# Kernel optimization log

Measured on AMD Instinct MI355X. Metric: run time of the kernel, lower is better.

The kernel has to match this reference:

```python
import jax, jax.numpy as jnp
import numpy as np

B, T, D, H = 4, 1024, 2048, 16
E = D // H  # head_dim = 128


def setup_inputs() -> dict:
    key = jax.random.key(0)
    ks = jax.random.split(key, 10)
    s = 1.0 / np.sqrt(D)
    x = jax.random.normal(ks[0], (B, T, D), dtype=jnp.float32)
    attention_mask = jnp.ones((B, T), dtype=jnp.int32)
    # Per-head q/k/v projections stacked along head axis: [H, E, D] weights, [H, E] biases.
    Wq = jax.random.uniform(ks[1], (H, E, D), jnp.float32, -s, s)
    bq = jax.random.uniform(ks[2], (H, E), jnp.float32, -s, s)
    Wk = jax.random.uniform(ks[3], (H, E, D), jnp.float32, -s, s)
    bk = jax.random.uniform(ks[4], (H, E), jnp.float32, -s, s)
    Wv = jax.random.uniform(ks[5], (H, E, D), jnp.float32, -s, s)
    bv = jax.random.uniform(ks[6], (H, E), jnp.float32, -s, s)
    Wo = jax.random.uniform(ks[7], (D, D), jnp.float32, -s, s)
    bo = jax.random.uniform(ks[8], (D,), jnp.float32, -s, s)
    return {"x": x, "attention_mask": attention_mask, "Wq": Wq, "bq": bq,
            "Wk": Wk, "bk": bk, "Wv": Wv, "bv": bv, "Wo": Wo, "bo": bo}


def _causal_mask(Tq, Tk, dtype):
    neg = jnp.finfo(dtype).min
    qi = jnp.arange(Tq)[:, None]
    ki = jnp.arange(Tk)[None, :]
    max_allowed = Tk - Tq + qi
    return jnp.where(ki > max_allowed, neg, jnp.zeros((), dtype)).astype(dtype)


def reference(x, attention_mask, Wq, bq, Wk, bk, Wv, bv, Wo, bo):
    dt = x.dtype
    neg = jnp.finfo(dt).min
    scale = 1.0 / np.sqrt(E)
    # per-head projections (vectorized over heads): [B,H,T,E]
    q = jnp.einsum('btd,hed->bhte', x, Wq) + bq[None, :, None, :]
    k = jnp.einsum('btd,hed->bhte', x, Wk) + bk[None, :, None, :]
    v = jnp.einsum('btd,hed->bhte', x, Wv) + bv[None, :, None, :]
    # scores [B,H,Tq,Tk]
    scores = jnp.einsum('bhqe,bhke->bhqk', q, k) * scale
    scores = scores + _causal_mask(T, T, dt)[None, None]
    keep = attention_mask.astype(bool)  # [B,Tk]
    scores = jnp.where(keep[:, None, None, :], scores, neg)
    probs = jax.nn.softmax(scores, axis=-1)
    y = jnp.einsum('bhqk,bhke->bhqe', probs, v)  # [B,H,T,E]
    # heads concatenated along feature dim in head order
    y = jnp.transpose(y, (0, 2, 1, 3)).reshape(B, T, D)
    out = y @ Wo.T + bo
    return out
```

## Files before the change

### kernel.cpp

```cpp
#include <hip/hip_runtime.h>
#include <hip/hip_bf16.h>


typedef __attribute__((ext_vector_type(4))) float f32x4;
typedef __attribute__((ext_vector_type(8))) short s16x8;
typedef __attribute__((ext_vector_type(4))) unsigned short us16x4;
typedef __attribute__((ext_vector_type(8))) unsigned short us16x8;

#define Td 1024
#define Dd 2048
#define SCALE 0.08838834764831845f

__device__ __forceinline__ unsigned short f2bf(float f) {
  unsigned int u = __builtin_bit_cast(unsigned int, f);
  u = (u + 0x7fffu + ((u >> 16) & 1u)) >> 16;
  return (unsigned short)u;
}

__device__ __forceinline__ void gload_lds16(const void* g, void* l) {
  __builtin_amdgcn_global_load_lds(
      (const __attribute__((address_space(1))) unsigned int*)g,
      (__attribute__((address_space(3))) unsigned int*)l, 16, 0, 0);
}

__global__ void cvt_f32_bf16(const float* __restrict__ in,
                             unsigned short* __restrict__ out, int n4) {
  int i = blockIdx.x * 256 + threadIdx.x;
  if (i >= n4) return;
  float4 v = reinterpret_cast<const float4*>(in)[i];
  us16x4 o = {f2bf(v.x), f2bf(v.y), f2bf(v.z), f2bf(v.w)};
  reinterpret_cast<us16x4*>(out)[i] = o;
}

__global__ void bias_concat(const float* __restrict__ bq, const float* __restrict__ bk,
                            const float* __restrict__ bv, float* __restrict__ out) {
  int i = blockIdx.x * 256 + threadIdx.x;
  const float* s = (i < 2048) ? bq : ((i < 4096) ? bk : bv);
  out[i] = s[i & 2047];
}

__global__ void prep_mask(const int* __restrict__ amask, unsigned* __restrict__ pmask) {
  const int b = blockIdx.x, tid = threadIdx.x;
  const int w = tid >> 6, lane = tid & 63;
#pragma unroll
  for (int j = 0; j < 4; ++j) {
    const int k = j * 256 + tid;
    unsigned long long ball = __ballot(amask[b * Td + k] != 0);
    if (lane == 0) {
      pmask[b * 32 + j * 8 + w * 2] = (unsigned)ball;
      pmask[b * 32 + j * 8 + w * 2 + 1] = (unsigned)(ball >> 32);
    }
  }
}

template <int MODE>
__global__ __launch_bounds__(256, 2) void gemm_bt(
    const unsigned short* __restrict__ A, const unsigned short* __restrict__ Bm,
    const float* __restrict__ bias, void* __restrict__ C,
    unsigned short* __restrict__ Cv, int M, int N, int K, int ldc) {
  __shared__ unsigned short As[8192];
  __shared__ unsigned short Bs[8192];
  const int tid = threadIdx.x;
  const int lane = tid & 63, w = tid >> 6;
  const int g = lane >> 4, m15 = lane & 15;
  const int wr = w >> 1, wc = w & 1;
  const int row0 = blockIdx.y * 128, col0 = blockIdx.x * 128;

  f32x4 acc[4][4] = {};
  const int nK = K >> 6;
  for (int kt = 0; kt < nK; ++kt) {
    const int k0 = kt << 6;
    __syncthreads();
#pragma unroll
    for (int i = 0; i < 4; ++i) {
      const int p = w * 256 + i * 64 + lane;
      const int prow = p >> 3;
      const int lslot = (p & 7) ^ (prow & 7);
      gload_lds16(A + (size_t)(row0 + prow) * K + k0 + lslot * 8,
                  &As[(size_t)(w * 256 + i * 64) * 8]);
      gload_lds16(Bm + (size_t)(col0 + prow) * K + k0 + lslot * 8,
                  &Bs[(size_t)(w * 256 + i * 64) * 8]);
    }
    __syncthreads();
#pragma unroll
    for (int ks = 0; ks < 2; ++ks) {
      s16x8 af[4], bf[4];
#pragma unroll
      for (int i = 0; i < 4; ++i) {
        const int r = wr * 64 + i * 16 + m15;
        af[i] = *reinterpret_cast<const s16x8*>(&As[(r * 8 + ((ks * 4 + g) ^ (r & 7))) * 8]);
      }
#pragma unroll
      for (int j = 0; j < 4; ++j) {
        const int r = wc * 64 + j * 16 + m15;
        bf[j] = *reinterpret_cast<const s16x8*>(&Bs[(r * 8 + ((ks * 4 + g) ^ (r & 7))) * 8]);
      }
#pragma unroll
      for (int i = 0; i < 4; ++i)
#pragma unroll
        for (int j = 0; j < 4; ++j)
          acc[i][j] = __builtin_amdgcn_mfma_f32_16x16x32_bf16(af[i], bf[j], acc[i][j], 0, 0, 0);
    }
  }
  if (MODE == 1 && col0 >= 4096) {
    const int vc0 = col0 - 4096;
#pragma unroll
    for (int j = 0; j < 4; ++j) {
      const int vcol = vc0 + wc * 64 + j * 16 + m15;
      const float bv = bias[4096 + vcol];
      const int hh = vcol >> 7, e = vcol & 127;
#pragma unroll
      for (int i = 0; i < 4; ++i) {
        const int row = row0 + wr * 64 + i * 16 + g * 4;
        const int bb = row >> 10, tt = row & 1023;
        us16x4 pk;
#pragma unroll
        for (int r = 0; r < 4; ++r) pk[r] = f2bf(acc[i][j][r] + bv);
        *reinterpret_cast<us16x4*>(&Cv[((size_t)((bb * 16 + hh) * 128 + e)) * Td + tt]) = pk;
      }
    }
  } else {
#pragma unroll
    for (int j = 0; j < 4; ++j) {
      const int col = col0 + wc * 64 + j * 16 + m15;
      const float bv = bias[col];
#pragma unroll
      for (int i = 0; i < 4; ++i)
#pragma unroll
        for (int r = 0; r < 4; ++r) {
          const int row = row0 + wr * 64 + i * 16 + g * 4 + r;
          const float v = acc[i][j][r] + bv;
          if (MODE)
            ((unsigned short*)C)[(size_t)row * ldc + col] = f2bf(v);
          else
            ((float*)C)[(size_t)row * ldc + col] = v;
        }
    }
  }
}

#define SOFTMAX_GRP(SV, G, QB, BND)                                              \
  {                                                                              \
    const int q = (QB) + m15;                                                    \
    float pv[16];                                                                \
    if (!(BND) && (pm0 & pm1) == 0xffffffffu) {                                  \
      _Pragma("unroll") for (int kc = 0; kc < 4; ++kc)                           \
          _Pragma("unroll") for (int r = 0; r < 4; ++r)                          \
              pv[kc * 4 + r] = SV[kc][r] * SCALE;                                \
    } else {                                                                     \
      _Pragma("unroll") for (int kc = 0; kc < 4; ++kc)                           \
          _Pragma("unroll") for (int r = 0; r < 4; ++r) {                        \
        const int kl = kc * 16 + g * 4 + r;                                      \
        const unsigned pmw = (kl < 32) ? pm0 : pm1;                              \
        const bool ok = ((pmw >> (kl & 31)) & 1u) && (k0 + kl <= q);             \
        pv[kc * 4 + r] = ok ? SV[kc][r] * SCALE : -3.0e38f;                      \
      }                                                                          \
    }                                                                            \
    float t0 = fmaxf(fmaxf(pv[0], pv[1]), fmaxf(pv[2], pv[3]));                  \
    float t1 = fmaxf(fmaxf(pv[4], pv[5]), fmaxf(pv[6], pv[7]));                  \
    float t2 = fmaxf(fmaxf(pv[8], pv[9]), fmaxf(pv[10], pv[11]));                \
    float t3 = fmaxf(fmaxf(pv[12], pv[13]), fmaxf(pv[14], pv[15]));              \
    float t = fmaxf(fmaxf(t0, t1), fmaxf(t2, t3));                               \
    t = fmaxf(t, __shfl_xor(t, 16));                                             \
    t = fmaxf(t, __shfl_xor(t, 32));                                             \
    const float mn = fmaxf(m_[G], t);                                            \
    const float al = __expf(m_[G] - mn);                                         \
    m_[G] = mn;                                                                  \
    float rs = 0.f;                                                              \
    _Pragma("unroll") for (int j = 0; j < 16; ++j) {                             \
      pv[j] = __expf(pv[j] - mn);                                                \
      rs += pv[j];                                                               \
    }                                                                            \
    rs += __shfl_xor(rs, 16);                                                    \
    rs += __shfl_xor(rs, 32);                                                    \
    l_[G] = l_[G] * al + rs;                                                     \
    _Pragma("unroll") for (int n = 0; n < 8; ++n) yt[G][n] *= al;                \
    _Pragma("unroll") for (int kc = 0; kc < 4; ++kc) {                           \
      us16x4 pk;                                                                 \
      _Pragma("unroll") for (int r = 0; r < 4; ++r) pk[r] = f2bf(pv[kc * 4 + r]);\
      const int ch = kc * 2 + (g >> 1);                                          \
      const int idx = (G) * 1024 + m15 * 64 + ((ch ^ (m15 & 7)) << 3) + (g & 1) * 4; \
      *reinterpret_cast<us16x4*>(&pw[idx]) = pk;                                 \
    }                                                                            \
  }

__global__ __launch_bounds__(512, 2) void attn(
    const unsigned short* __restrict__ qk, const unsigned short* __restrict__ vt,
    const unsigned* __restrict__ pmask, unsigned short* __restrict__ Y) {
  __shared__ unsigned short Ks[2][8192];
  __shared__ unsigned short Vs[2][8192];
  __shared__ unsigned short Ps[8][2048];
  const int d = blockIdx.x;
  const int slot = d >> 3;
  const int bh = (d & 7) * 8 + (slot >> 2);
  const int p = slot & 3;
  const int b = bh >> 4, h = bh & 15;
  const int ta = p, tb = 7 - p;
  const int tid = threadIdx.x, lane = tid & 63, w = tid >> 6;
  const int g = lane >> 4, m15 = lane & 15;
  const int qa = ta * 128 + w * 16, qb = tb * 128 + w * 16;
  unsigned short* pw = Ps[w];

  const unsigned short* qkb = qk + (size_t)b * Td * 4096;
  const unsigned short* vbb = vt + (size_t)bh * 128 * Td;

  s16x8 qf[2][4];
#pragma unroll
  for (int G = 0; G < 2; ++G) {
    const int q_ = G ? qb : qa;
#pragma unroll
    for (int c = 0; c < 4; ++c)
      qf[G][c] = *reinterpret_cast<const s16x8*>(
          &qkb[(size_t)(q_ + m15) * 4096 + h * 128 + c * 32 + g * 8]);
  }

  f32x4 yt[2][8] = {};
  float m_[2] = {-3.0e38f, -3.0e38f}, l_[2] = {0.f, 0.f};

  auto stage = [&](int buf, int kt) {
    const int k0s = kt << 6;
#pragma unroll
    for (int i = 0; i < 2; ++i) {
      const int pc = i * 512 + tid;
      const int kr = pc >> 4, ch = pc & 15;
      const int ls = ch ^ (kr & 7);
      gload_lds16(qkb + (size_t)(k0s + kr) * 4096 + 2048 + h * 128 + ls * 8,
                  &Ks[buf][(i * 512 + w * 64) * 8]);
      const int e = pc >> 3, cv = pc & 7;
      const int vs = cv ^ (e & 7);
      gload_lds16(vbb + (size_t)e * Td + k0s + vs * 8,
                  &Vs[buf][(i * 512 + w * 64) * 8]);
    }
  };

  const int nA = 2 * ta + 2, nB = 2 * tb + 2;
  stage(0, 0);
  asm volatile("s_waitcnt vmcnt(0)" ::: "memory");
  __syncthreads();
  int cur = 0;
  for (int kt = 0; kt < nB; ++kt) {
    const int k0 = kt << 6;
    const bool actA = kt < nA;
    if (kt + 1 < nB) stage(cur ^ 1, kt + 1);
    const unsigned pm0 = pmask[b * 32 + kt * 2];
    const unsigned pm1 = pmask[b * 32 + kt * 2 + 1];

    f32x4 s0[4] = {}, s1[4] = {};
    __builtin_amdgcn_s_setprio(1);
#pragma unroll
    for (int kc = 0; kc < 4; ++kc) {
      const int krow = kc * 16 + m15;
#pragma unroll
      for (int c = 0; c < 4; ++c) {
        const s16x8 kf = *reinterpret_cast<const s16x8*>(
            &Ks[cur][krow * 128 + (((c * 4 + g) ^ (krow & 7))) * 8]);
        if (actA) s0[kc] = __builtin_amdgcn_mfma_f32_16x16x32_bf16(kf, qf[0][c], s0[kc], 0, 0, 0);
        s1[kc] = __builtin_amdgcn_mfma_f32_16x16x32_bf16(kf, qf[1][c], s1[kc], 0, 0, 0);
      }
    }
    __builtin_amdgcn_s_setprio(0);

    if (actA) SOFTMAX_GRP(s0, 0, qa, kt >= 2 * ta)
    SOFTMAX_GRP(s1, 1, qb, kt >= 2 * tb)

    asm volatile("s_waitcnt lgkmcnt(0)" ::: "memory");
    __builtin_amdgcn_sched_barrier(0);
    s16x8 pf0[2], pf1[2];
#pragma unroll
    for (int kcc = 0; kcc < 2; ++kcc) {
      if (actA)
        pf0[kcc] = *reinterpret_cast<const s16x8*>(
            &pw[m15 * 64 + (((kcc * 4 + g) ^ (m15 & 7))) * 8]);
      pf1[kcc] = *reinterpret_cast<const s16x8*>(
          &pw[1024 + m15 * 64 + (((kcc * 4 + g) ^ (m15 & 7))) * 8]);
    }

    __builtin_amdgcn_s_setprio(1);
#pragma unroll
    for (int nt = 0; nt < 8; ++nt) {
      const int e = nt * 16 + m15;
#pragma unroll
      for (int kcc = 0; kcc < 2; ++kcc) {
        const s16x8 vf = *reinterpret_cast<const s16x8*>(
            &Vs[cur][e * 64 + (((kcc * 4 + g) ^ (e & 7))) * 8]);
        if (actA) yt[0][nt] = __builtin_amdgcn_mfma_f32_16x16x32_bf16(vf, pf0[kcc], yt[0][nt], 0, 0, 0);
        yt[1][nt] = __builtin_amdgcn_mfma_f32_16x16x32_bf16(vf, pf1[kcc], yt[1][nt], 0, 0, 0);
      }
    }
    __builtin_amdgcn_s_setprio(0);

    asm volatile("s_waitcnt vmcnt(0)" ::: "memory");
    __syncthreads();
    cur ^= 1;
  }

#pragma unroll
  for (int G = 0; G < 2; ++G) {
    const int q_ = G ? qb : qa;
    const float inv = 1.0f / l_[G];
#pragma unroll
    for (int half = 0; half < 2; ++half) {
#pragma unroll
      for (int ntl = 0; ntl < 4; ++ntl) {
        const int nt = half * 4 + ntl;
        us16x4 pk;
#pragma unroll
        for (int r = 0; r < 4; ++r) pk[r] = f2bf(yt[G][nt][r] * inv);
        const int slot8 = ntl * 4 + g;
        const int idx = m15 * 64 + (((slot8 >> 1) ^ (m15 & 7))) * 8 + (slot8 & 1) * 4;
        *reinterpret_cast<us16x4*>(&pw[idx]) = pk;
      }
      asm volatile("s_waitcnt lgkmcnt(0)" ::: "memory");
      __builtin_amdgcn_sched_barrier(0);
      const int qq = lane >> 2, c4 = lane & 3;
#pragma unroll
      for (int rr = 0; rr < 2; ++rr) {
        const int pr = c4 + rr * 4;
        us16x8 vv = *reinterpret_cast<const us16x8*>(&pw[qq * 64 + ((pr ^ (qq & 7))) * 8]);
        *reinterpret_cast<us16x8*>(
            &Y[(size_t)(b * Td + q_ + qq) * Dd + h * 128 + half * 64 + pr * 8]) = vv;
      }
      asm volatile("s_waitcnt lgkmcnt(0)" ::: "memory");
      __builtin_amdgcn_sched_barrier(0);
    }
  }
}

extern "C" void kernel_launch(void* const* d_in, const int* in_sizes, int n_in,
                              void* d_out, int out_size, void* d_ws, size_t ws_size,
                              hipStream_t stream) {
  const float* x = (const float*)d_in[0];
  const int* amask = (const int*)d_in[1];
  const float* Wq = (const float*)d_in[2];
  const float* bq = (const float*)d_in[3];
  const float* Wk = (const float*)d_in[4];
  const float* bk = (const float*)d_in[5];
  const float* Wv = (const float*)d_in[6];
  const float* bv = (const float*)d_in[7];
  const float* Wo = (const float*)d_in[8];
  const float* bo = (const float*)d_in[9];
  float* out = (float*)d_out;

  char* ws = (char*)d_ws;
  unsigned short* wqkv = (unsigned short*)(ws);
  unsigned short* xbf  = (unsigned short*)(ws + 25165824);
  unsigned short* qk   = (unsigned short*)(ws + 41943040);
  unsigned short* vt   = (unsigned short*)(ws + 75497472);
  unsigned short* wobf = (unsigned short*)(ws + 92274688);
  float* bqkv          = (float*)(ws + 100663296);
  unsigned short* ybuf = xbf;
  unsigned* pmask      = (unsigned*)ws;

  cvt_f32_bf16<<<8192, 256, 0, stream>>>(x, xbf, 2097152);
  cvt_f32_bf16<<<4096, 256, 0, stream>>>(Wq, wqkv, 1048576);
  cvt_f32_bf16<<<4096, 256, 0, stream>>>(Wk, wqkv + 4194304, 1048576);
  cvt_f32_bf16<<<4096, 256, 0, stream>>>(Wv, wqkv + 8388608, 1048576);
  cvt_f32_bf16<<<4096, 256, 0, stream>>>(Wo, wobf, 1048576);
  bias_concat<<<24, 256, 0, stream>>>(bq, bk, bv, bqkv);

  gemm_bt<1><<<dim3(48, 32), 256, 0, stream>>>(xbf, wqkv, bqkv, (void*)qk, vt, 4096, 6144, 2048, 4096);
  prep_mask<<<4, 256, 0, stream>>>(amask, pmask);
  attn<<<256, 512, 0, stream>>>(qk, vt, pmask, ybuf);
  gemm_bt<0><<<dim3(16, 32), 256, 0, stream>>>(ybuf, wobf, bo, (void*)out, nullptr, 4096, 2048, 2048, 2048);
}
```

Before: 352.1 us.

## Split QKV GEMM into three launches and halve attention query tiles

The fused QKV projection GEMM becomes three separate launches (Q, K, and V with a transposed-output mode), each writing through a column offset. The attention kernel moves from 512-thread blocks covering two 128-row query tiles to 256-thread blocks covering two 64-row tiles, with twice as many blocks, paired for causal load balance. The goal is finer-grained attention work and better occupancy across CUs. The cost is extra launch overhead and more redundant K/V staging per block.

```diff
diff --git a/kernel.cpp b/kernel.cpp
--- a/kernel.cpp
+++ b/kernel.cpp
@@ -57,7 +57,7 @@
 __global__ __launch_bounds__(256, 2) void gemm_bt(
     const unsigned short* __restrict__ A, const unsigned short* __restrict__ Bm,
     const float* __restrict__ bias, void* __restrict__ C,
-    unsigned short* __restrict__ Cv, int M, int N, int K, int ldc) {
+    unsigned short* __restrict__ Cv, int M, int N, int K, int ldc, int coloff) {
   __shared__ unsigned short As[8192];
   __shared__ unsigned short Bs[8192];
   const int tid = threadIdx.x;
@@ -102,12 +102,11 @@
           acc[i][j] = __builtin_amdgcn_mfma_f32_16x16x32_bf16(af[i], bf[j], acc[i][j], 0, 0, 0);
     }
   }
-  if (MODE == 1 && col0 >= 4096) {
-    const int vc0 = col0 - 4096;
+  if (MODE == 2) {
 #pragma unroll
     for (int j = 0; j < 4; ++j) {
-      const int vcol = vc0 + wc * 64 + j * 16 + m15;
-      const float bv = bias[4096 + vcol];
+      const int vcol = col0 + wc * 64 + j * 16 + m15;
+      const float bv = bias[vcol];
       const int hh = vcol >> 7, e = vcol & 127;
 #pragma unroll
       for (int i = 0; i < 4; ++i) {
@@ -122,8 +121,8 @@
   } else {
 #pragma unroll
     for (int j = 0; j < 4; ++j) {
-      const int col = col0 + wc * 64 + j * 16 + m15;
-      const float bv = bias[col];
+      const int coll = col0 + wc * 64 + j * 16 + m15;
+      const float bv = bias[coll];
 #pragma unroll
       for (int i = 0; i < 4; ++i)
 #pragma unroll
@@ -131,9 +130,9 @@
           const int row = row0 + wr * 64 + i * 16 + g * 4 + r;
           const float v = acc[i][j][r] + bv;
           if (MODE)
-            ((unsigned short*)C)[(size_t)row * ldc + col] = f2bf(v);
+            ((unsigned short*)C)[(size_t)row * ldc + coloff + coll] = f2bf(v);
           else
-            ((float*)C)[(size_t)row * ldc + col] = v;
+            ((float*)C)[(size_t)row * ldc + coll] = v;
         }
     }
   }
@@ -184,21 +183,23 @@
     }                                                                            \
   }
 
-__global__ __launch_bounds__(512, 2) void attn(
+__global__ __launch_bounds__(256, 2) void attn(
     const unsigned short* __restrict__ qk, const unsigned short* __restrict__ vt,
     const unsigned* __restrict__ pmask, unsigned short* __restrict__ Y) {
   __shared__ unsigned short Ks[2][8192];
   __shared__ unsigned short Vs[2][8192];
-  __shared__ unsigned short Ps[8][2048];
+  __shared__ unsigned short Ps[4][2048];
   const int d = blockIdx.x;
-  const int slot = d >> 3;
-  const int bh = (d & 7) * 8 + (slot >> 2);
-  const int p = slot & 3;
+  const int half = d >> 8, r_ = d & 255;
+  const int praw = r_ >> 6;
+  const int p = half ? (7 - praw) : praw;
+  const int bhx = r_ & 63;
+  const int bh = (bhx & 7) * 8 + (bhx >> 3);
   const int b = bh >> 4, h = bh & 15;
-  const int ta = p, tb = 7 - p;
+  const int ta = p, tb = 15 - p;
   const int tid = threadIdx.x, lane = tid & 63, w = tid >> 6;
   const int g = lane >> 4, m15 = lane & 15;
-  const int qa = ta * 128 + w * 16, qb = tb * 128 + w * 16;
+  const int qa = ta * 64 + w * 16, qb = tb * 64 + w * 16;
   unsigned short* pw = Ps[w];
 
   const unsigned short* qkb = qk + (size_t)b * Td * 4096;
@@ -220,28 +221,28 @@
   auto stage = [&](int buf, int kt) {
     const int k0s = kt << 6;
 #pragma unroll
-    for (int i = 0; i < 2; ++i) {
-      const int pc = i * 512 + tid;
+    for (int i = 0; i < 4; ++i) {
+      const int pc = i * 256 + tid;
       const int kr = pc >> 4, ch = pc & 15;
       const int ls = ch ^ (kr & 7);
       gload_lds16(qkb + (size_t)(k0s + kr) * 4096 + 2048 + h * 128 + ls * 8,
-                  &Ks[buf][(i * 512 + w * 64) * 8]);
+                  &Ks[buf][(i * 256 + w * 64) * 8]);
       const int e = pc >> 3, cv = pc & 7;
       const int vs = cv ^ (e & 7);
       gload_lds16(vbb + (size_t)e * Td + k0s + vs * 8,
-                  &Vs[buf][(i * 512 + w * 64) * 8]);
+                  &Vs[buf][(i * 256 + w * 64) * 8]);
     }
   };
 
-  const int nA = 2 * ta + 2, nB = 2 * tb + 2;
+  const int nkt = tb + 1;
   stage(0, 0);
   asm volatile("s_waitcnt vmcnt(0)" ::: "memory");
   __syncthreads();
   int cur = 0;
-  for (int kt = 0; kt < nB; ++kt) {
+  for (int kt = 0; kt < nkt; ++kt) {
     const int k0 = kt << 6;
-    const bool actA = kt < nA;
-    if (kt + 1 < nB) stage(cur ^ 1, kt + 1);
+    const bool actA = (kt <= ta);
+    if (kt + 1 < nkt) stage(cur ^ 1, kt + 1);
     const unsigned pm0 = pmask[b * 32 + kt * 2];
     const unsigned pm1 = pmask[b * 32 + kt * 2 + 1];
 
@@ -260,8 +261,8 @@
     }
     __builtin_amdgcn_s_setprio(0);
 
-    if (actA) SOFTMAX_GRP(s0, 0, qa, kt >= 2 * ta)
-    SOFTMAX_GRP(s1, 1, qb, kt >= 2 * tb)
+    if (actA) SOFTMAX_GRP(s0, 0, qa, kt == ta)
+    SOFTMAX_GRP(s1, 1, qb, kt == tb)
 
     asm volatile("s_waitcnt lgkmcnt(0)" ::: "memory");
     __builtin_amdgcn_sched_barrier(0);
@@ -299,10 +300,10 @@
     const int q_ = G ? qb : qa;
     const float inv = 1.0f / l_[G];
 #pragma unroll
-    for (int half = 0; half < 2; ++half) {
+    for (int hf = 0; hf < 2; ++hf) {
 #pragma unroll
       for (int ntl = 0; ntl < 4; ++ntl) {
-        const int nt = half * 4 + ntl;
+        const int nt = hf * 4 + ntl;
         us16x4 pk;
 #pragma unroll
         for (int r = 0; r < 4; ++r) pk[r] = f2bf(yt[G][nt][r] * inv);
@@ -318,7 +319,7 @@
         const int pr = c4 + rr * 4;
         us16x8 vv = *reinterpret_cast<const us16x8*>(&pw[qq * 64 + ((pr ^ (qq & 7))) * 8]);
         *reinterpret_cast<us16x8*>(
-            &Y[(size_t)(b * Td + q_ + qq) * Dd + h * 128 + half * 64 + pr * 8]) = vv;
+            &Y[(size_t)(b * Td + q_ + qq) * Dd + h * 128 + hf * 64 + pr * 8]) = vv;
       }
       asm volatile("s_waitcnt lgkmcnt(0)" ::: "memory");
       __builtin_amdgcn_sched_barrier(0);
@@ -358,8 +359,14 @@
   cvt_f32_bf16<<<4096, 256, 0, stream>>>(Wo, wobf, 1048576);
   bias_concat<<<24, 256, 0, stream>>>(bq, bk, bv, bqkv);
 
-  gemm_bt<1><<<dim3(48, 32), 256, 0, stream>>>(xbf, wqkv, bqkv, (void*)qk, vt, 4096, 6144, 2048, 4096);
+  gemm_bt<1><<<dim3(16, 32), 256, 0, stream>>>(xbf, wqkv, bqkv, (void*)qk, nullptr,
+                                               4096, 2048, 2048, 4096, 0);
+  gemm_bt<1><<<dim3(16, 32), 256, 0, stream>>>(xbf, wqkv + 4194304, bqkv + 2048, (void*)qk,
+                                               nullptr, 4096, 2048, 2048, 4096, 2048);
+  gemm_bt<2><<<dim3(16, 32), 256, 0, stream>>>(xbf, wqkv + 8388608, bqkv + 4096, nullptr,
+                                               vt, 4096, 2048, 2048, 4096, 0);
   prep_mask<<<4, 256, 0, stream>>>(amask, pmask);
-  attn<<<256, 512, 0, stream>>>(qk, vt, pmask, ybuf);
-  gemm_bt<0><<<dim3(16, 32), 256, 0, stream>>>(ybuf, wobf, bo, (void*)out, nullptr, 4096, 2048, 2048, 2048);
-}
+  attn<<<512, 256, 0, stream>>>(qk, vt, pmask, ybuf);
+  gemm_bt<0><<<dim3(16, 32), 256, 0, stream>>>(ybuf, wobf, bo, (void*)out, nullptr,
+                                               4096, 2048, 2048, 2048, 0);
+}
```

New measurement: 362.8 us. 3.0% more time.
